# Kernel tuning notes

Measured on AMD Instinct MI355X. Metric: run time of the kernel, lower is better.

## Reference

```python
import jax, jax.numpy as jnp
import numpy as np

B, T, Z, S, H = 32, 128, 100, 6, 64
F1, F2 = 512, 128


def setup_inputs() -> dict:
    key = jax.random.key(0)
    ks = jax.random.split(key, 11)
    g = lambda k, shape, sc: (jax.random.normal(k, shape, dtype=jnp.float32) * sc)
    return {
        "x": jax.random.normal(ks[0], (B, T, Z, S), dtype=jnp.float32),
        "W_ih": g(ks[1], (3 * H, S), 0.125),   # GRU input weights [r|z|n]
        "W_hh": g(ks[2], (3 * H, H), 0.125),   # GRU hidden weights [r|z|n]
        "b_ih": g(ks[3], (3 * H,), 0.125),
        "b_hh": g(ks[4], (3 * H,), 0.125),
        "w1": g(ks[5], (F1, H), 0.1),
        "b1": g(ks[6], (F1,), 0.1),
        "w2": g(ks[7], (F2, F1), 0.04),
        "b2": g(ks[8], (F2,), 0.04),
        "w3": g(ks[9], (1, F2), 0.09),
        "b3": g(ks[10], (1,), 0.09),
    }


def reference(x, W_ih, W_hh, b_ih, b_hh, w1, b1, w2, b2, w3, b3):
    b, t, z, s = x.shape
    h_dim = W_hh.shape[1]
    # Fuse the per-zone python loop into the batch dim, zone-major so the
    # final reshape matches torch.stack(a).view(-1, t, nzones).
    xm = jnp.transpose(x, (2, 0, 1, 3)).reshape(z * b, t, s)  # (ZB, T, S)
    # Precompute input projections for all timesteps (one big GEMM).
    gi_all = jnp.einsum('nts,gs->ntg', xm, W_ih) + b_ih        # (ZB, T, 3H)

    def step(h, gi):
        gh = h @ W_hh.T + b_hh
        r = jax.nn.sigmoid(gi[:, :h_dim] + gh[:, :h_dim])
        zg = jax.nn.sigmoid(gi[:, h_dim:2 * h_dim] + gh[:, h_dim:2 * h_dim])
        n = jnp.tanh(gi[:, 2 * h_dim:] + r * gh[:, 2 * h_dim:])
        h_new = (1.0 - zg) * n + zg * h
        return h_new, h_new

    h0 = jnp.zeros((z * b, h_dim), x.dtype)
    _, sx = jax.lax.scan(step, h0, jnp.swapaxes(gi_all, 0, 1))  # (T, ZB, H)
    sx = jnp.swapaxes(sx, 0, 1)                                  # (ZB, T, H)

    a1 = jax.nn.relu(sx @ w1.T + b1)
    a2 = jax.nn.relu(a1 @ w2.T + b2)
    a3 = a2 @ w3.T + b3                                          # (ZB, T, 1)
    return a3.reshape(-1, t, z)                                  # (B, T, Z)
```

## Files before the change

kernel.cpp:

```cpp
#include <hip/hip_runtime.h>
#include <stdint.h>

#define Tdim 128
#define Zdim 100
#define Sdim 6
#define Hdim 64
#define ZB   3200
#define F1   512
#define F2   128
#define Mrows (ZB * Tdim)

typedef _Float16 f16x8 __attribute__((ext_vector_type(8)));
typedef _Float16 f16x4 __attribute__((ext_vector_type(4)));
typedef float f32x4 __attribute__((ext_vector_type(4)));
typedef uint32_t u32x4 __attribute__((ext_vector_type(4)));

__device__ __forceinline__ float sigmoidf_fast(float x) {
  return 1.f / (1.f + __expf(-x));
}
__device__ __forceinline__ float tanhf_fast(float x) {
  return 1.f - 2.f / (__expf(2.f * x) + 1.f);
}

__global__ __launch_bounds__(256) void prep_kernel(
    const float* __restrict__ W_ih, const float* __restrict__ W_hh,
    const float* __restrict__ w1, const float* __restrict__ w2,
    _Float16* __restrict__ Wf, _Float16* __restrict__ w1p,
    _Float16* __restrict__ w2p) {
  int i = blockIdx.x * 256 + threadIdx.x;
  if (i < 192 * 96) {
    int g = i / 96, k = i - g * 96;
    float v = (k < 64) ? W_hh[g * 64 + k] : ((k < 70) ? W_ih[g * 6 + (k - 64)] : 0.f);
    Wf[i] = (_Float16)v;
  }
  int j = i - 192 * 96;
  if (j >= 0 && j < 32768) {
    int kt = j >> 11, ntl = (j >> 10) & 1, kf = (j >> 9) & 1;
    int lane = (j >> 3) & 63, e = j & 7;
    int q = lane >> 4, c = lane & 15;
    int row = kt * 32 + ntl * 16 + c;
    int h = kf * 32 + q * 8 + e;
    w1p[j] = (_Float16)w1[row * 64 + h];
  }
  int l = j - 32768;
  if (l >= 0 && l < 65536) {
    int kt = l >> 12, nt = (l >> 9) & 7;
    int lane = (l >> 3) & 63, e = l & 7;
    int q = lane >> 4, c = lane & 15;
    int row = nt * 16 + c;
    int k = kt * 32 + q * 8 + e;
    w2p[l] = (_Float16)w2[row * 512 + k];
  }
}

__global__ __launch_bounds__(256, 1) void gru_kernel(
    const float* __restrict__ x, const _Float16* __restrict__ Wf,
    const float* __restrict__ b_ih, const float* __restrict__ b_hh,
    _Float16* __restrict__ sx) {
  __shared__ __align__(16) _Float16 hist[32][16][72];
  __shared__ __align__(16) _Float16 xs[Tdim][16][8];
  const int tid = threadIdx.x;
  const int lane = tid & 63;
  const int w = tid >> 6;
  const int c = lane & 15;
  const int q = lane >> 4;

  for (int i = 0; i < 8; i++) {
    int idx = i * 256 + tid;
    int t = idx >> 4, row = idx & 15;
    int nr = blockIdx.x * 16 + row;
    const float* p = x + (size_t)(nr & 31) * (Tdim * Zdim * Sdim)
                       + (size_t)t * (Zdim * Sdim) + (size_t)(nr >> 5) * Sdim;
    f16x8 v;
    v[0] = (_Float16)p[0]; v[1] = (_Float16)p[1]; v[2] = (_Float16)p[2];
    v[3] = (_Float16)p[3]; v[4] = (_Float16)p[4]; v[5] = (_Float16)p[5];
    v[6] = (_Float16)0.f;  v[7] = (_Float16)0.f;
    *(f16x8*)&xs[t][row][0] = v;
  }

  const int gr0 = w * 16;
  const int gz0 = 64 + w * 16;
  const int gn0 = 128 + w * 16;

  f16x8 Ar[3], Az[3], Anh[2], Ani;
#pragma unroll
  for (int kf = 0; kf < 3; kf++) {
    Ar[kf] = *(const f16x8*)(Wf + (size_t)(gr0 + c) * 96 + kf * 32 + q * 8);
    Az[kf] = *(const f16x8*)(Wf + (size_t)(gz0 + c) * 96 + kf * 32 + q * 8);
  }
  Anh[0] = *(const f16x8*)(Wf + (size_t)(gn0 + c) * 96 + q * 8);
  Anh[1] = *(const f16x8*)(Wf + (size_t)(gn0 + c) * 96 + 32 + q * 8);
  Ani    = *(const f16x8*)(Wf + (size_t)(gn0 + c) * 96 + 64 + q * 8);

  f32x4 Cr, Cz, Cnh, Cni;
  {
    f32x4 bir = *(const f32x4*)(b_ih + gr0 + q * 4);
    f32x4 bhr = *(const f32x4*)(b_hh + gr0 + q * 4);
    f32x4 biz = *(const f32x4*)(b_ih + gz0 + q * 4);
    f32x4 bhz = *(const f32x4*)(b_hh + gz0 + q * 4);
#pragma unroll
    for (int r = 0; r < 4; r++) { Cr[r] = bir[r] + bhr[r]; Cz[r] = biz[r] + bhz[r]; }
    Cnh = *(const f32x4*)(b_hh + gn0 + q * 4);
    Cni = *(const f32x4*)(b_ih + gn0 + q * 4);
  }

  __syncthreads();

  f16x8 Bh0 = {0, 0, 0, 0, 0, 0, 0, 0};
  f16x8 Bh1 = {0, 0, 0, 0, 0, 0, 0, 0};
  f32x4 hprev = {0.f, 0.f, 0.f, 0.f};

  f32x4 Dr_s, Dz_s, Dni_s;
  {
    f16x8 xv8 = *(const f16x8*)&xs[0][c][0];
    f16x8 Bx;
#pragma unroll
    for (int j = 0; j < 8; j++) Bx[j] = (q == 0) ? xv8[j] : (_Float16)0.f;
    Dni_s = __builtin_amdgcn_mfma_f32_16x16x32_f16(Ani, Bx, Cni, 0, 0, 0);
    Dr_s  = __builtin_amdgcn_mfma_f32_16x16x32_f16(Ar[2], Bx, Cr, 0, 0, 0);
    Dz_s  = __builtin_amdgcn_mfma_f32_16x16x32_f16(Az[2], Bx, Cz, 0, 0, 0);
  }

#pragma unroll 1
  for (int tch = 0; tch < 4; tch++) {
#pragma unroll 1
    for (int tc = 0; tc < 32; tc++) {
      const int t = tch * 32 + tc;
      f32x4 Dnh = __builtin_amdgcn_mfma_f32_16x16x32_f16(Anh[0], Bh0, Cnh, 0, 0, 0);
      f32x4 Dr  = __builtin_amdgcn_mfma_f32_16x16x32_f16(Ar[0], Bh0, Dr_s, 0, 0, 0);
      f32x4 Dz  = __builtin_amdgcn_mfma_f32_16x16x32_f16(Az[0], Bh0, Dz_s, 0, 0, 0);
      Dnh = __builtin_amdgcn_mfma_f32_16x16x32_f16(Anh[1], Bh1, Dnh, 0, 0, 0);
      Dr  = __builtin_amdgcn_mfma_f32_16x16x32_f16(Ar[1], Bh1, Dr, 0, 0, 0);
      Dz  = __builtin_amdgcn_mfma_f32_16x16x32_f16(Az[1], Bh1, Dz, 0, 0, 0);

      f16x4 pk;
#pragma unroll
      for (int r = 0; r < 4; r++) {
        float rr = sigmoidf_fast(Dr[r]);
        float zg = sigmoidf_fast(Dz[r]);
        float nn = tanhf_fast(Dni_s[r] + rr * Dnh[r]);
        float hnew = nn + zg * (hprev[r] - nn);
        hprev[r] = hnew;
        pk[r] = (_Float16)hnew;
      }
      *(f16x4*)&hist[tc][c][w * 16 + q * 4] = pk;

      if (t + 1 < Tdim) {
        f16x8 xv8 = *(const f16x8*)&xs[t + 1][c][0];
        f16x8 Bx;
#pragma unroll
        for (int j = 0; j < 8; j++) Bx[j] = (q == 0) ? xv8[j] : (_Float16)0.f;
        Dni_s = __builtin_amdgcn_mfma_f32_16x16x32_f16(Ani, Bx, Cni, 0, 0, 0);
        Dr_s  = __builtin_amdgcn_mfma_f32_16x16x32_f16(Ar[2], Bx, Cr, 0, 0, 0);
        Dz_s  = __builtin_amdgcn_mfma_f32_16x16x32_f16(Az[2], Bx, Cz, 0, 0, 0);
      }
      __syncthreads();
      Bh0 = *(const f16x8*)&hist[tc][c][q * 8];
      Bh1 = *(const f16x8*)&hist[tc][c][32 + q * 8];
    }
    {
      const int t0 = tch * 32;
#pragma unroll
      for (int rr2 = 0; rr2 < 4; rr2++) {
        const int row = w * 4 + rr2;
        const int nrow = blockIdx.x * 16 + row;
        _Float16* dst = sx + (size_t)nrow * Tdim * Hdim + (size_t)t0 * Hdim;
#pragma unroll
        for (int it = 0; it < 4; it++) {
          int idx = it * 64 + lane;
          int tcc = idx >> 3, hd8 = idx & 7;
          f16x8 vv = *(const f16x8*)&hist[tcc][row][hd8 * 8];
          *(f16x8*)(dst + tcc * 64 + hd8 * 8) = vv;
        }
      }
      __syncthreads();
    }
  }
}

__global__ __launch_bounds__(256, 2) void mlp_kernel(
    const _Float16* __restrict__ sx, const _Float16* __restrict__ w1p,
    const _Float16* __restrict__ w2p, const float* __restrict__ b1,
    const float* __restrict__ b2, const float* __restrict__ w3,
    const float* __restrict__ b3, float* __restrict__ out) {
  __shared__ __align__(16) _Float16 w1s[2][2048];
  __shared__ __align__(16) _Float16 w2s[2][4096];
  __shared__ __align__(16) _Float16 rep[4][4][512];
  const int tid = threadIdx.x;
  const int lane = tid & 63;
  const int wave = tid >> 6;
  const int c = lane & 15;
  const int q = lane >> 4;
  const size_t m0 = ((size_t)blockIdx.x * 4 + wave) * 64;

  f16x8 Bs[4][2];
#pragma unroll
  for (int g = 0; g < 4; g++)
#pragma unroll
    for (int kk = 0; kk < 2; kk++)
      Bs[g][kk] = *(const f16x8*)(sx + (m0 + g * 16 + c) * Hdim + kk * 32 + q * 8);

  f32x4 acc2[4][8];
#pragma unroll
  for (int g = 0; g < 4; g++)
#pragma unroll
    for (int nt = 0; nt < 8; nt++) acc2[g][nt] = (f32x4){0.f, 0.f, 0.f, 0.f};

  u32x4 r1, r2a, r2b;
  {
    const u32x4* g1 = (const u32x4*)(w1p);
    const u32x4* g2 = (const u32x4*)(w2p);
    r1 = g1[tid];
    r2a = g2[tid];
    r2b = g2[256 + tid];
    ((u32x4*)&w1s[0][0])[tid] = r1;
    ((u32x4*)&w2s[0][0])[tid] = r2a;
    ((u32x4*)&w2s[0][0])[256 + tid] = r2b;
  }
  __syncthreads();

#pragma unroll 1
  for (int kt = 0; kt < 16; kt++) {
    const int buf = kt & 1;
    if (kt + 1 < 16) {
      const u32x4* g1 = (const u32x4*)(w1p + (size_t)(kt + 1) * 2048);
      const u32x4* g2 = (const u32x4*)(w2p + (size_t)(kt + 1) * 4096);
      r1 = g1[tid];
      r2a = g2[tid];
      r2b = g2[256 + tid];
    }

#pragma unroll
    for (int ntl = 0; ntl < 2; ntl++) {
      const int f1b = kt * 32 + ntl * 16;
      f16x8 A0 = *(const f16x8*)&w1s[buf][ntl * 1024 + lane * 8];
      f16x8 A1 = *(const f16x8*)&w1s[buf][ntl * 1024 + 512 + lane * 8];
      f32x4 bb = *(const f32x4*)(b1 + f1b + q * 4);
      const int roff = ((2 * ntl + (q >> 1)) * 16 + c) * 8 + (q & 1) * 4;
#pragma unroll
      for (int g = 0; g < 4; g++) {
        f32x4 cc = __builtin_amdgcn_mfma_f32_16x16x32_f16(A0, Bs[g][0], bb, 0, 0, 0);
        cc = __builtin_amdgcn_mfma_f32_16x16x32_f16(A1, Bs[g][1], cc, 0, 0, 0);
        f16x4 pk;
#pragma unroll
        for (int r = 0; r < 4; r++)
          pk[r] = (_Float16)(cc[r] > 0.f ? cc[r] : 0.f);
        *(f16x4*)&rep[wave][g][roff] = pk;
      }
    }
    f16x8 Ba[4];
#pragma unroll
    for (int g = 0; g < 4; g++)
      Ba[g] = *(const f16x8*)&rep[wave][g][lane * 8];
#pragma unroll
    for (int nt = 0; nt < 8; nt++) {
      f16x8 A2 = *(const f16x8*)&w2s[buf][nt * 512 + lane * 8];
#pragma unroll
      for (int g = 0; g < 4; g++)
        acc2[g][nt] = __builtin_amdgcn_mfma_f32_16x16x32_f16(A2, Ba[g], acc2[g][nt], 0, 0, 0);
    }

    if (kt + 1 < 16) {
      ((u32x4*)&w1s[buf ^ 1][0])[tid] = r1;
      ((u32x4*)&w2s[buf ^ 1][0])[tid] = r2a;
      ((u32x4*)&w2s[buf ^ 1][0])[256 + tid] = r2b;
      __syncthreads();
    }
  }

  float part[4] = {0.f, 0.f, 0.f, 0.f};
#pragma unroll
  for (int nt = 0; nt < 8; nt++) {
    f32x4 bb = *(const f32x4*)(b2 + nt * 16 + q * 4);
    f32x4 ww = *(const f32x4*)(w3 + nt * 16 + q * 4);
#pragma unroll
    for (int g = 0; g < 4; g++) {
#pragma unroll
      for (int r = 0; r < 4; r++) {
        float v = acc2[g][nt][r] + bb[r];
        v = v > 0.f ? v : 0.f;
        part[g] = fmaf(v, ww[r], part[g]);
      }
    }
  }
#pragma unroll
  for (int g = 0; g < 4; g++) {
    part[g] += __shfl_xor(part[g], 16, 64);
    part[g] += __shfl_xor(part[g], 32, 64);
  }
  float pv = (q == 0) ? part[0] : (q == 1) ? part[1] : (q == 2) ? part[2] : part[3];
  out[m0 + q * 16 + c] = pv + b3[0];
}

extern "C" void kernel_launch(void* const* d_in, const int* in_sizes, int n_in,
                              void* d_out, int out_size, void* d_ws, size_t ws_size,
                              hipStream_t stream) {
  const float* x    = (const float*)d_in[0];
  const float* W_ih = (const float*)d_in[1];
  const float* W_hh = (const float*)d_in[2];
  const float* b_ih = (const float*)d_in[3];
  const float* b_hh = (const float*)d_in[4];
  const float* w1   = (const float*)d_in[5];
  const float* b1   = (const float*)d_in[6];
  const float* w2   = (const float*)d_in[7];
  const float* b2   = (const float*)d_in[8];
  const float* w3   = (const float*)d_in[9];
  const float* b3   = (const float*)d_in[10];
  float* out = (float*)d_out;

  char* ws = (char*)d_ws;
  _Float16* sxf = (_Float16*)ws;
  _Float16* Wf  = (_Float16*)(ws + 52428800);
  _Float16* w1p = (_Float16*)(ws + 52428800 + 36864);
  _Float16* w2p = (_Float16*)(ws + 52428800 + 36864 + 65536);

  hipLaunchKernelGGL(prep_kernel, dim3(456), dim3(256), 0, stream,
                     W_ih, W_hh, w1, w2, Wf, w1p, w2p);
  hipLaunchKernelGGL(gru_kernel, dim3(ZB / 16), dim3(256), 0, stream,
                     x, Wf, b_ih, b_hh, sxf);
  hipLaunchKernelGGL(mlp_kernel, dim3(Mrows / 256), dim3(256), 0, stream,
                     sxf, w1p, w2p, b1, b2, w3, b3, out);
}
```

Before: 255.0 us.

## Process two independent 16-row chains per GRU block to hide MFMA latency

New measurement: 350.8 us. +37.6%, slower.

```diff
diff --git a/kernel.cpp b/kernel.cpp
--- a/kernel.cpp
+++ b/kernel.cpp
@@ -57,18 +57,18 @@
     const float* __restrict__ x, const _Float16* __restrict__ Wf,
     const float* __restrict__ b_ih, const float* __restrict__ b_hh,
     _Float16* __restrict__ sx) {
-  __shared__ __align__(16) _Float16 hist[32][16][72];
-  __shared__ __align__(16) _Float16 xs[Tdim][16][8];
+  __shared__ __align__(16) _Float16 hist[16][32][72];
+  __shared__ __align__(16) _Float16 xs[Tdim][32][8];
   const int tid = threadIdx.x;
   const int lane = tid & 63;
   const int w = tid >> 6;
   const int c = lane & 15;
   const int q = lane >> 4;
 
-  for (int i = 0; i < 8; i++) {
+  for (int i = 0; i < 16; i++) {
     int idx = i * 256 + tid;
-    int t = idx >> 4, row = idx & 15;
-    int nr = blockIdx.x * 16 + row;
+    int t = idx >> 5, row = idx & 31;
+    int nr = blockIdx.x * 32 + row;
     const float* p = x + (size_t)(nr & 31) * (Tdim * Zdim * Sdim)
                        + (size_t)t * (Zdim * Sdim) + (size_t)(nr >> 5) * Sdim;
     f16x8 v;
@@ -106,67 +106,81 @@
 
   __syncthreads();
 
-  f16x8 Bh0 = {0, 0, 0, 0, 0, 0, 0, 0};
-  f16x8 Bh1 = {0, 0, 0, 0, 0, 0, 0, 0};
-  f32x4 hprev = {0.f, 0.f, 0.f, 0.f};
-
-  f32x4 Dr_s, Dz_s, Dni_s;
-  {
-    f16x8 xv8 = *(const f16x8*)&xs[0][c][0];
+  f16x8 Bh0[2], Bh1[2];
+  f32x4 hprev[2];
+  f32x4 Dr_s[2], Dz_s[2], Dni_s[2];
+  const f32x4 zero4 = {0.f, 0.f, 0.f, 0.f};
+#pragma unroll
+  for (int ch = 0; ch < 2; ch++) {
+    Bh0[ch] = (f16x8){0, 0, 0, 0, 0, 0, 0, 0};
+    Bh1[ch] = (f16x8){0, 0, 0, 0, 0, 0, 0, 0};
+    hprev[ch] = zero4;
+    f16x8 xv8 = *(const f16x8*)&xs[0][ch * 16 + c][0];
     f16x8 Bx;
 #pragma unroll
     for (int j = 0; j < 8; j++) Bx[j] = (q == 0) ? xv8[j] : (_Float16)0.f;
-    Dni_s = __builtin_amdgcn_mfma_f32_16x16x32_f16(Ani, Bx, Cni, 0, 0, 0);
-    Dr_s  = __builtin_amdgcn_mfma_f32_16x16x32_f16(Ar[2], Bx, Cr, 0, 0, 0);
-    Dz_s  = __builtin_amdgcn_mfma_f32_16x16x32_f16(Az[2], Bx, Cz, 0, 0, 0);
+    Dni_s[ch] = __builtin_amdgcn_mfma_f32_16x16x32_f16(Ani, Bx, Cni, 0, 0, 0);
+    Dr_s[ch]  = __builtin_amdgcn_mfma_f32_16x16x32_f16(Ar[2], Bx, Cr, 0, 0, 0);
+    Dz_s[ch]  = __builtin_amdgcn_mfma_f32_16x16x32_f16(Az[2], Bx, Cz, 0, 0, 0);
   }
 
 #pragma unroll 1
-  for (int tch = 0; tch < 4; tch++) {
+  for (int tch = 0; tch < 8; tch++) {
 #pragma unroll 1
-    for (int tc = 0; tc < 32; tc++) {
-      const int t = tch * 32 + tc;
-      f32x4 Dnh = __builtin_amdgcn_mfma_f32_16x16x32_f16(Anh[0], Bh0, Cnh, 0, 0, 0);
-      f32x4 Dr  = __builtin_amdgcn_mfma_f32_16x16x32_f16(Ar[0], Bh0, Dr_s, 0, 0, 0);
-      f32x4 Dz  = __builtin_amdgcn_mfma_f32_16x16x32_f16(Az[0], Bh0, Dz_s, 0, 0, 0);
-      Dnh = __builtin_amdgcn_mfma_f32_16x16x32_f16(Anh[1], Bh1, Dnh, 0, 0, 0);
-      Dr  = __builtin_amdgcn_mfma_f32_16x16x32_f16(Ar[1], Bh1, Dr, 0, 0, 0);
-      Dz  = __builtin_amdgcn_mfma_f32_16x16x32_f16(Az[1], Bh1, Dz, 0, 0, 0);
-
-      f16x4 pk;
-#pragma unroll
-      for (int r = 0; r < 4; r++) {
-        float rr = sigmoidf_fast(Dr[r]);
-        float zg = sigmoidf_fast(Dz[r]);
-        float nn = tanhf_fast(Dni_s[r] + rr * Dnh[r]);
-        float hnew = nn + zg * (hprev[r] - nn);
-        hprev[r] = hnew;
-        pk[r] = (_Float16)hnew;
-      }
-      *(f16x4*)&hist[tc][c][w * 16 + q * 4] = pk;
-
+    for (int tc = 0; tc < 16; tc++) {
+      const int t = tch * 16 + tc;
+      f32x4 dnh0[2], dr0[2], dz0[2], dnh1[2], dr1[2], dz1[2];
+#pragma unroll
+      for (int ch = 0; ch < 2; ch++) {
+        dnh0[ch] = __builtin_amdgcn_mfma_f32_16x16x32_f16(Anh[0], Bh0[ch], Cnh, 0, 0, 0);
+        dr0[ch]  = __builtin_amdgcn_mfma_f32_16x16x32_f16(Ar[0], Bh0[ch], Dr_s[ch], 0, 0, 0);
+        dz0[ch]  = __builtin_amdgcn_mfma_f32_16x16x32_f16(Az[0], Bh0[ch], Dz_s[ch], 0, 0, 0);
+        dnh1[ch] = __builtin_amdgcn_mfma_f32_16x16x32_f16(Anh[1], Bh1[ch], zero4, 0, 0, 0);
+        dr1[ch]  = __builtin_amdgcn_mfma_f32_16x16x32_f16(Ar[1], Bh1[ch], zero4, 0, 0, 0);
+        dz1[ch]  = __builtin_amdgcn_mfma_f32_16x16x32_f16(Az[1], Bh1[ch], zero4, 0, 0, 0);
+      }
+#pragma unroll
+      for (int ch = 0; ch < 2; ch++) {
+        f16x4 pk;
+#pragma unroll
+        for (int r = 0; r < 4; r++) {
+          float rr = sigmoidf_fast(dr0[ch][r] + dr1[ch][r]);
+          float zg = sigmoidf_fast(dz0[ch][r] + dz1[ch][r]);
+          float nn = tanhf_fast(Dni_s[ch][r] + rr * (dnh0[ch][r] + dnh1[ch][r]));
+          float hnew = nn + zg * (hprev[ch][r] - nn);
+          hprev[ch][r] = hnew;
+          pk[r] = (_Float16)hnew;
+        }
+        *(f16x4*)&hist[tc][ch * 16 + c][w * 16 + q * 4] = pk;
+      }
       if (t + 1 < Tdim) {
-        f16x8 xv8 = *(const f16x8*)&xs[t + 1][c][0];
-        f16x8 Bx;
-#pragma unroll
-        for (int j = 0; j < 8; j++) Bx[j] = (q == 0) ? xv8[j] : (_Float16)0.f;
-        Dni_s = __builtin_amdgcn_mfma_f32_16x16x32_f16(Ani, Bx, Cni, 0, 0, 0);
-        Dr_s  = __builtin_amdgcn_mfma_f32_16x16x32_f16(Ar[2], Bx, Cr, 0, 0, 0);
-        Dz_s  = __builtin_amdgcn_mfma_f32_16x16x32_f16(Az[2], Bx, Cz, 0, 0, 0);
+#pragma unroll
+        for (int ch = 0; ch < 2; ch++) {
+          f16x8 xv8 = *(const f16x8*)&xs[t + 1][ch * 16 + c][0];
+          f16x8 Bx;
+#pragma unroll
+          for (int j = 0; j < 8; j++) Bx[j] = (q == 0) ? xv8[j] : (_Float16)0.f;
+          Dni_s[ch] = __builtin_amdgcn_mfma_f32_16x16x32_f16(Ani, Bx, Cni, 0, 0, 0);
+          Dr_s[ch]  = __builtin_amdgcn_mfma_f32_16x16x32_f16(Ar[2], Bx, Cr, 0, 0, 0);
+          Dz_s[ch]  = __builtin_amdgcn_mfma_f32_16x16x32_f16(Az[2], Bx, Cz, 0, 0, 0);
+        }
       }
       __syncthreads();
-      Bh0 = *(const f16x8*)&hist[tc][c][q * 8];
-      Bh1 = *(const f16x8*)&hist[tc][c][32 + q * 8];
+#pragma unroll
+      for (int ch = 0; ch < 2; ch++) {
+        Bh0[ch] = *(const f16x8*)&hist[tc][ch * 16 + c][q * 8];
+        Bh1[ch] = *(const f16x8*)&hist[tc][ch * 16 + c][32 + q * 8];
+      }
     }
     {
-      const int t0 = tch * 32;
-#pragma unroll
-      for (int rr2 = 0; rr2 < 4; rr2++) {
-        const int row = w * 4 + rr2;
-        const int nrow = blockIdx.x * 16 + row;
+      const int t0 = tch * 16;
+#pragma unroll
+      for (int rr2 = 0; rr2 < 8; rr2++) {
+        const int row = w * 8 + rr2;
+        const int nrow = blockIdx.x * 32 + row;
         _Float16* dst = sx + (size_t)nrow * Tdim * Hdim + (size_t)t0 * Hdim;
 #pragma unroll
-        for (int it = 0; it < 4; it++) {
+        for (int it = 0; it < 2; it++) {
           int idx = it * 64 + lane;
           int tcc = idx >> 3, hd8 = idx & 7;
           f16x8 vv = *(const f16x8*)&hist[tcc][row][hd8 * 8];
@@ -316,7 +330,7 @@
 
   hipLaunchKernelGGL(prep_kernel, dim3(456), dim3(256), 0, stream,
                      W_ih, W_hh, w1, w2, Wf, w1p, w2p);
-  hipLaunchKernelGGL(gru_kernel, dim3(ZB / 16), dim3(256), 0, stream,
+  hipLaunchKernelGGL(gru_kernel, dim3(ZB / 32), dim3(256), 0, stream,
                      x, Wf, b_ih, b_hh, sxf);
   hipLaunchKernelGGL(mlp_kernel, dim3(Mrows / 256), dim3(256), 0, stream,
                      sxf, w1p, w2p, b1, b2, w3, b3, out);
```
